# Kernel tuning notes

Measured on AMD Instinct MI355X. Metric: run time of the kernel, lower is better.

## Reference

```python
import jax, jax.numpy as jnp
import numpy as np

N_CAR, N_LIGHT, N_STOP = 180000, 10000, 10000
N = N_CAR + N_LIGHT + N_STOP
E = 6_400_000

# LossConfig defaults
LAMBDA_RECON, LAMBDA_RULE, LAMBDA_ATTN, LAMBDA_REG = 1.0, 0.5, 0.3, 1e-4
W_ATTN_GAT, W_ATTN_RULE = 0.5, 0.5
VIOL_THRESH = 0.5


def setup_inputs() -> dict:
    key = jax.random.key(0)
    ks = jax.random.split(key, 8)
    eps = 1e-6
    model_scores = jnp.clip(jax.random.uniform(ks[0], (N_CAR,), jnp.float32), eps, 1.0 - eps)
    rule_scores = jnp.clip(jax.random.uniform(ks[1], (N_CAR,), jnp.float32), eps, 1.0 - eps)
    alpha_gat = jax.random.uniform(ks[2], (E,), jnp.float32)
    beta_rule = jax.random.uniform(ks[3], (N_CAR,), jnp.float32)
    src = jax.random.randint(ks[4], (E,), 0, N)
    dst = jax.random.randint(ks[5], (E,), 0, N)
    edge_index = jnp.stack([src, dst], axis=0)
    # cars first (type 0), then lights (1), then stop lines (2)
    entity_types = jnp.concatenate([
        jnp.zeros((N_CAR,), jnp.int32),
        jnp.ones((N_LIGHT,), jnp.int32),
        jnp.full((N_STOP,), 2, jnp.int32),
    ])
    param0 = jax.random.normal(ks[6], (4096, 4096), jnp.float32) * 0.02
    param1 = jax.random.normal(ks[7], (4096, 4096), jnp.float32) * 0.02
    return {
        "model_scores": model_scores, "rule_scores": rule_scores,
        "alpha_gat": alpha_gat, "beta_rule": beta_rule,
        "edge_index": edge_index, "entity_types": entity_types,
        "param0": param0, "param1": param1,
    }


def _bce(x, t):
    # torch F.binary_cross_entropy clamps log at -100
    log_x = jnp.clip(jnp.log(x), -100.0)
    log_1mx = jnp.clip(jnp.log1p(-x), -100.0)
    return jnp.mean(-(t * log_x + (1.0 - t) * log_1mx))


def _gat_attn_loss(alpha_gat, edge_index, entity_types, violation_mask):
    src, dst = edge_index[0], edge_index[1]
    dst_t = entity_types[dst]
    rule_edge = (dst_t == 1) | (dst_t == 2)
    masked = jnp.where(rule_edge, alpha_gat, -jnp.inf)
    # fused segment-max over source nodes replaces the per-car Python loop
    seg_max = jax.ops.segment_max(masked, src, num_segments=N)  # [N]
    car_ids = jnp.nonzero(entity_types == 0, size=N_CAR)[0]      # [N_car]
    max_attn = seg_max[car_ids]                                  # [N_car]
    valid = jnp.isfinite(max_attn) & violation_mask             # cars w/ rule neighbor
    safe = jnp.where(valid, max_attn, 0.0)
    total = jnp.sum(jnp.where(valid, (1.0 - safe) ** 2, 0.0))
    cnt = jnp.sum(valid)
    return jnp.where(cnt > 0, total / jnp.maximum(cnt, 1).astype(total.dtype), 0.0)


def _rule_attn_loss(beta_rule, violation_mask):
    total = jnp.sum(jnp.where(violation_mask, (1.0 - beta_rule) ** 2, 0.0))
    cnt = jnp.sum(violation_mask)
    return jnp.where(cnt > 0, total / jnp.maximum(cnt, 1).astype(total.dtype), 0.0)


@jax.jit
def reference(model_scores, rule_scores, alpha_gat, beta_rule, edge_index, entity_types, param0, param1):
    L_recon = _bce(model_scores, rule_scores)
    L_rule = jnp.mean((model_scores - rule_scores) ** 2)
    violation_mask = rule_scores > VIOL_THRESH
    any_viol = jnp.any(violation_mask)
    L_attn_gat = jnp.where(any_viol, _gat_attn_loss(alpha_gat, edge_index, entity_types, violation_mask), 0.0)
    L_attn_rule = jnp.where(any_viol, _rule_attn_loss(beta_rule, violation_mask), 0.0)
    L_attn = W_ATTN_GAT * L_attn_gat + W_ATTN_RULE * L_attn_rule
    L_reg = jnp.sum(param0 ** 2) + jnp.sum(param1 ** 2)
    L_total = (LAMBDA_RECON * L_recon + LAMBDA_RULE * L_rule
               + LAMBDA_ATTN * L_attn + LAMBDA_REG * L_reg)
    num_violations = jnp.sum(violation_mask).astype(jnp.float32)
    return (L_total, L_recon, L_rule, L_attn, L_attn_gat, L_attn_rule, L_reg, num_violations)
```

## Files before the change

kernel.cpp:

```cpp
#include <hip/hip_runtime.h>

#define N_CAR   180000
#define NE      6400000
#define P_ELEMS (4096 * 4096)
#define P4      (P_ELEMS / 4)

#define REG_BLOCKS   2048
#define REG_THREADS  (REG_BLOCKS * 256)
#define REG_ITERS    (P4 / REG_THREADS)

#define EDGE_BLOCKS  2048
#define EDGE_THREADS (EDGE_BLOCKS * 256)
#define EDGE_QUADS   (NE / 4)

#define CAR_BLOCKS   ((N_CAR + 255) / 256)

typedef float f4 __attribute__((ext_vector_type(4)));
typedef int   i4 __attribute__((ext_vector_type(4)));


__device__ __forceinline__ float wave_reduce_sum(float s) {
#pragma unroll
    for (int off = 32; off > 0; off >>= 1) s += __shfl_down(s, off, 64);
    return s;
}

__global__ void __launch_bounds__(256) init_kernel(i4* __restrict__ segmax4) {
    int i = blockIdx.x * blockDim.x + threadIdx.x;
    const int NINF = (int)0xFF800000u;
    if (i < N_CAR / 4) {
        i4 v = {NINF, NINF, NINF, NINF};
        segmax4[i] = v;
    }
}

__global__ void __launch_bounds__(256) fused_kernel(const i4* __restrict__ src4,
                                                    const i4* __restrict__ dst4,
                                                    const f4* __restrict__ alpha4,
                                                    int* __restrict__ segmax,
                                                    const f4* __restrict__ p0,
                                                    const f4* __restrict__ p1,
                                                    float* __restrict__ regpart) {
    __shared__ float red[4];
    int slot = blockIdx.x & 1;
    int g    = blockIdx.x >> 1;
    if (slot == 0) {
        int t = g * 256 + threadIdx.x;
        f4 acc = {0.f, 0.f, 0.f, 0.f};
#pragma unroll
        for (int k = 0; k < REG_ITERS; ++k) {
            f4 a = p0[t + k * REG_THREADS];
            acc += a * a;
        }
#pragma unroll
        for (int k = 0; k < REG_ITERS; ++k) {
            f4 b = p1[t + k * REG_THREADS];
            acc += b * b;
        }
        float s = (acc.x + acc.y) + (acc.z + acc.w);
        s = wave_reduce_sum(s);
        int wave = threadIdx.x >> 6;
        int lane = threadIdx.x & 63;
        if (lane == 0) red[wave] = s;
        __syncthreads();
        if (threadIdx.x == 0)
            regpart[g] = red[0] + red[1] + red[2] + red[3];
    } else {
        int t = g * 256 + threadIdx.x;
        for (int q = t; q < EDGE_QUADS; q += EDGE_THREADS) {
            i4 d  = dst4[q];
            i4 sv = src4[q];
            f4 a  = alpha4[q];
            if (d.x >= N_CAR && sv.x < N_CAR) atomicMax(&segmax[sv.x], __float_as_int(a.x));
            if (d.y >= N_CAR && sv.y < N_CAR) atomicMax(&segmax[sv.y], __float_as_int(a.y));
            if (d.z >= N_CAR && sv.z < N_CAR) atomicMax(&segmax[sv.z], __float_as_int(a.z));
            if (d.w >= N_CAR && sv.w < N_CAR) atomicMax(&segmax[sv.w], __float_as_int(a.w));
        }
    }
}

__global__ void __launch_bounds__(256) car_kernel(const float* __restrict__ ms,
                                                  const float* __restrict__ rs,
                                                  const float* __restrict__ beta,
                                                  const int* __restrict__ segmax,
                                                  float* __restrict__ carpart) {
    int i = blockIdx.x * blockDim.x + threadIdx.x;
    float vals[6] = {0.f, 0.f, 0.f, 0.f, 0.f, 0.f};
    if (i < N_CAR) {
        float x = ms[i];
        float t = rs[i];
        float lx  = fmaxf(logf(x), -100.0f);
        float l1x = fmaxf(log1pf(-x), -100.0f);
        vals[0] = -(t * lx + (1.0f - t) * l1x);
        float df = x - t;
        vals[1] = df * df;
        if (t > 0.5f) {
            vals[2] = 1.0f;
            float b = beta[i];
            vals[3] = (1.0f - b) * (1.0f - b);
            float m = __int_as_float(segmax[i]);
            if (m >= 0.0f) {
                vals[4] = (1.0f - m) * (1.0f - m);
                vals[5] = 1.0f;
            }
        }
    }
    __shared__ float red[4][6];
    int wave = threadIdx.x >> 6;
    int lane = threadIdx.x & 63;
#pragma unroll
    for (int k = 0; k < 6; ++k) {
        float s = wave_reduce_sum(vals[k]);
        if (lane == 0) red[wave][k] = s;
    }
    __syncthreads();
    if (threadIdx.x == 0) {
#pragma unroll
        for (int k = 0; k < 6; ++k)
            carpart[blockIdx.x * 6 + k] = red[0][k] + red[1][k] + red[2][k] + red[3][k];
    }
}

__global__ void __launch_bounds__(256) finalize_kernel(const float* __restrict__ regpart,
                                                       const float* __restrict__ carpart,
                                                       float* __restrict__ out) {
    int tid = threadIdx.x;
    float rsum = 0.0f;
    for (int i = tid; i < REG_BLOCKS; i += 256) rsum += regpart[i];
    float c[6] = {0.f, 0.f, 0.f, 0.f, 0.f, 0.f};
    for (int r = tid; r < CAR_BLOCKS; r += 256) {
#pragma unroll
        for (int k = 0; k < 6; ++k) c[k] += carpart[r * 6 + k];
    }
    __shared__ float red[4][7];
    int wave = tid >> 6;
    int lane = tid & 63;
    {
        float s = wave_reduce_sum(rsum);
        if (lane == 0) red[wave][6] = s;
    }
#pragma unroll
    for (int k = 0; k < 6; ++k) {
        float s = wave_reduce_sum(c[k]);
        if (lane == 0) red[wave][k] = s;
    }
    __syncthreads();
    if (tid == 0) {
        float tot[7];
#pragma unroll
        for (int k = 0; k < 7; ++k)
            tot[k] = red[0][k] + red[1][k] + red[2][k] + red[3][k];
        const float inv_ncar = 1.0f / (float)N_CAR;
        float L_recon = tot[0] * inv_ncar;
        float L_rule  = tot[1] * inv_ncar;
        float vc      = tot[2];
        float L_attn_rule = (vc > 0.0f) ? tot[3] / vc : 0.0f;
        float gat_cnt = tot[5];
        float L_attn_gat = (vc > 0.0f && gat_cnt > 0.0f) ? tot[4] / gat_cnt : 0.0f;
        float L_attn = 0.5f * L_attn_gat + 0.5f * L_attn_rule;
        float L_reg  = tot[6];
        float L_total = 1.0f * L_recon + 0.5f * L_rule + 0.3f * L_attn + 1e-4f * L_reg;
        out[0] = L_total;
        out[1] = L_recon;
        out[2] = L_rule;
        out[3] = L_attn;
        out[4] = L_attn_gat;
        out[5] = L_attn_rule;
        out[6] = L_reg;
        out[7] = vc;
    }
}

extern "C" void kernel_launch(void* const* d_in, const int* in_sizes, int n_in,
                              void* d_out, int out_size, void* d_ws, size_t ws_size,
                              hipStream_t stream) {
    const float* model_scores = (const float*)d_in[0];
    const float* rule_scores  = (const float*)d_in[1];
    const float* alpha_gat    = (const float*)d_in[2];
    const float* beta_rule    = (const float*)d_in[3];
    const int*   edge_index   = (const int*)d_in[4];
    const float* param0       = (const float*)d_in[6];
    const float* param1       = (const float*)d_in[7];
    float* out = (float*)d_out;

    int*   segmax  = (int*)d_ws;
    float* regpart = (float*)d_ws + N_CAR;
    float* carpart = regpart + REG_BLOCKS;

    const int* src = edge_index;
    const int* dst = edge_index + NE;

    init_kernel<<<(N_CAR / 4 + 255) / 256, 256, 0, stream>>>((i4*)segmax);
    fused_kernel<<<REG_BLOCKS + EDGE_BLOCKS, 256, 0, stream>>>(
        (const i4*)src, (const i4*)dst, (const f4*)alpha_gat, segmax,
        (const f4*)param0, (const f4*)param1, regpart);
    car_kernel<<<CAR_BLOCKS, 256, 0, stream>>>(model_scores, rule_scores,
                                               beta_rule, segmax, carpart);
    finalize_kernel<<<1, 256, 0, stream>>>(regpart, carpart, out);
}
```

Baseline: 233.2 us.

## Merge reg and edge work per block, fold finalize into car kernel via atomics

Each of the 4096 blocks now does its slice of the parameter sum of squares and then its slice of the edge atomicMax scan, instead of splitting blocks between the two jobs. The partial sums are accumulated with global atomicAdd. A last-block ticket in the car kernel computes the final losses, which removes the separate finalize launch. This saves one kernel launch and the partial-sum arrays, but it adds atomic contention on the accumulators and makes the float summation order nondeterministic.

Measured after the change: 293.9 us. +26.0%, slower.

```diff
diff --git a/kernel.cpp b/kernel.cpp
--- a/kernel.cpp
+++ b/kernel.cpp
@@ -5,12 +5,9 @@
 #define P_ELEMS (4096 * 4096)
 #define P4      (P_ELEMS / 4)
 
-#define REG_BLOCKS   2048
-#define REG_THREADS  (REG_BLOCKS * 256)
-#define REG_ITERS    (P4 / REG_THREADS)
-
-#define EDGE_BLOCKS  2048
-#define EDGE_THREADS (EDGE_BLOCKS * 256)
+#define WORK_BLOCKS  4096
+#define WORK_T       (WORK_BLOCKS * 256)
+#define REG_ITERS    (P4 / WORK_T)
 #define EDGE_QUADS   (NE / 4)
 
 #define CAR_BLOCKS   ((N_CAR + 255) / 256)
@@ -25,65 +22,65 @@
     return s;
 }
 
-__global__ void __launch_bounds__(256) init_kernel(i4* __restrict__ segmax4) {
+__global__ void __launch_bounds__(256) init_kernel(i4* __restrict__ segmax4,
+                                                   float* __restrict__ acc,
+                                                   int* __restrict__ done) {
     int i = blockIdx.x * blockDim.x + threadIdx.x;
     const int NINF = (int)0xFF800000u;
     if (i < N_CAR / 4) {
         i4 v = {NINF, NINF, NINF, NINF};
         segmax4[i] = v;
     }
+    if (i < 7) acc[i] = 0.0f;
+    if (i == 7) *done = 0;
 }
 
-__global__ void __launch_bounds__(256) fused_kernel(const i4* __restrict__ src4,
-                                                    const i4* __restrict__ dst4,
-                                                    const f4* __restrict__ alpha4,
-                                                    int* __restrict__ segmax,
-                                                    const f4* __restrict__ p0,
-                                                    const f4* __restrict__ p1,
-                                                    float* __restrict__ regpart) {
+__global__ void __launch_bounds__(256) work_kernel(const i4* __restrict__ src4,
+                                                   const i4* __restrict__ dst4,
+                                                   const f4* __restrict__ alpha4,
+                                                   int* __restrict__ segmax,
+                                                   const f4* __restrict__ p0,
+                                                   const f4* __restrict__ p1,
+                                                   float* __restrict__ acc) {
+    int t = blockIdx.x * 256 + threadIdx.x;
+    f4 a = {0.f, 0.f, 0.f, 0.f};
+#pragma unroll
+    for (int k = 0; k < REG_ITERS; ++k) {
+        f4 v = p0[t + k * WORK_T];
+        a += v * v;
+    }
+#pragma unroll
+    for (int k = 0; k < REG_ITERS; ++k) {
+        f4 v = p1[t + k * WORK_T];
+        a += v * v;
+    }
+    float s = (a.x + a.y) + (a.z + a.w);
+    s = wave_reduce_sum(s);
     __shared__ float red[4];
-    int slot = blockIdx.x & 1;
-    int g    = blockIdx.x >> 1;
-    if (slot == 0) {
-        int t = g * 256 + threadIdx.x;
-        f4 acc = {0.f, 0.f, 0.f, 0.f};
-#pragma unroll
-        for (int k = 0; k < REG_ITERS; ++k) {
-            f4 a = p0[t + k * REG_THREADS];
-            acc += a * a;
-        }
-#pragma unroll
-        for (int k = 0; k < REG_ITERS; ++k) {
-            f4 b = p1[t + k * REG_THREADS];
-            acc += b * b;
-        }
-        float s = (acc.x + acc.y) + (acc.z + acc.w);
-        s = wave_reduce_sum(s);
-        int wave = threadIdx.x >> 6;
-        int lane = threadIdx.x & 63;
-        if (lane == 0) red[wave] = s;
-        __syncthreads();
-        if (threadIdx.x == 0)
-            regpart[g] = red[0] + red[1] + red[2] + red[3];
-    } else {
-        int t = g * 256 + threadIdx.x;
-        for (int q = t; q < EDGE_QUADS; q += EDGE_THREADS) {
-            i4 d  = dst4[q];
-            i4 sv = src4[q];
-            f4 a  = alpha4[q];
-            if (d.x >= N_CAR && sv.x < N_CAR) atomicMax(&segmax[sv.x], __float_as_int(a.x));
-            if (d.y >= N_CAR && sv.y < N_CAR) atomicMax(&segmax[sv.y], __float_as_int(a.y));
-            if (d.z >= N_CAR && sv.z < N_CAR) atomicMax(&segmax[sv.z], __float_as_int(a.z));
-            if (d.w >= N_CAR && sv.w < N_CAR) atomicMax(&segmax[sv.w], __float_as_int(a.w));
-        }
+    int wave = threadIdx.x >> 6;
+    int lane = threadIdx.x & 63;
+    if (lane == 0) red[wave] = s;
+    __syncthreads();
+    if (threadIdx.x == 0)
+        atomicAdd(&acc[6], red[0] + red[1] + red[2] + red[3]);
+    for (int q = t; q < EDGE_QUADS; q += WORK_T) {
+        i4 d  = dst4[q];
+        i4 sv = src4[q];
+        f4 al = alpha4[q];
+        if (d.x >= N_CAR && sv.x < N_CAR) atomicMax(&segmax[sv.x], __float_as_int(al.x));
+        if (d.y >= N_CAR && sv.y < N_CAR) atomicMax(&segmax[sv.y], __float_as_int(al.y));
+        if (d.z >= N_CAR && sv.z < N_CAR) atomicMax(&segmax[sv.z], __float_as_int(al.z));
+        if (d.w >= N_CAR && sv.w < N_CAR) atomicMax(&segmax[sv.w], __float_as_int(al.w));
     }
 }
 
-__global__ void __launch_bounds__(256) car_kernel(const float* __restrict__ ms,
-                                                  const float* __restrict__ rs,
-                                                  const float* __restrict__ beta,
-                                                  const int* __restrict__ segmax,
-                                                  float* __restrict__ carpart) {
+__global__ void __launch_bounds__(256) carfin_kernel(const float* __restrict__ ms,
+                                                     const float* __restrict__ rs,
+                                                     const float* __restrict__ beta,
+                                                     const int* __restrict__ segmax,
+                                                     float* __restrict__ acc,
+                                                     int* __restrict__ done,
+                                                     float* __restrict__ out) {
     int i = blockIdx.x * blockDim.x + threadIdx.x;
     float vals[6] = {0.f, 0.f, 0.f, 0.f, 0.f, 0.f};
     if (i < N_CAR) {
@@ -117,57 +114,33 @@
     if (threadIdx.x == 0) {
 #pragma unroll
         for (int k = 0; k < 6; ++k)
-            carpart[blockIdx.x * 6 + k] = red[0][k] + red[1][k] + red[2][k] + red[3][k];
-    }
-}
-
-__global__ void __launch_bounds__(256) finalize_kernel(const float* __restrict__ regpart,
-                                                       const float* __restrict__ carpart,
-                                                       float* __restrict__ out) {
-    int tid = threadIdx.x;
-    float rsum = 0.0f;
-    for (int i = tid; i < REG_BLOCKS; i += 256) rsum += regpart[i];
-    float c[6] = {0.f, 0.f, 0.f, 0.f, 0.f, 0.f};
-    for (int r = tid; r < CAR_BLOCKS; r += 256) {
+            atomicAdd(&acc[k], red[0][k] + red[1][k] + red[2][k] + red[3][k]);
+        __threadfence();
+        int ticket = atomicAdd(done, 1);
+        if (ticket == CAR_BLOCKS - 1) {
+            float tot[7];
 #pragma unroll
-        for (int k = 0; k < 6; ++k) c[k] += carpart[r * 6 + k];
-    }
-    __shared__ float red[4][7];
-    int wave = tid >> 6;
-    int lane = tid & 63;
-    {
-        float s = wave_reduce_sum(rsum);
-        if (lane == 0) red[wave][6] = s;
-    }
-#pragma unroll
-    for (int k = 0; k < 6; ++k) {
-        float s = wave_reduce_sum(c[k]);
-        if (lane == 0) red[wave][k] = s;
-    }
-    __syncthreads();
-    if (tid == 0) {
-        float tot[7];
-#pragma unroll
-        for (int k = 0; k < 7; ++k)
-            tot[k] = red[0][k] + red[1][k] + red[2][k] + red[3][k];
-        const float inv_ncar = 1.0f / (float)N_CAR;
-        float L_recon = tot[0] * inv_ncar;
-        float L_rule  = tot[1] * inv_ncar;
-        float vc      = tot[2];
-        float L_attn_rule = (vc > 0.0f) ? tot[3] / vc : 0.0f;
-        float gat_cnt = tot[5];
-        float L_attn_gat = (vc > 0.0f && gat_cnt > 0.0f) ? tot[4] / gat_cnt : 0.0f;
-        float L_attn = 0.5f * L_attn_gat + 0.5f * L_attn_rule;
-        float L_reg  = tot[6];
-        float L_total = 1.0f * L_recon + 0.5f * L_rule + 0.3f * L_attn + 1e-4f * L_reg;
-        out[0] = L_total;
-        out[1] = L_recon;
-        out[2] = L_rule;
-        out[3] = L_attn;
-        out[4] = L_attn_gat;
-        out[5] = L_attn_rule;
-        out[6] = L_reg;
-        out[7] = vc;
+            for (int k = 0; k < 7; ++k)
+                tot[k] = atomicAdd(&acc[k], 0.0f);
+            const float inv_ncar = 1.0f / (float)N_CAR;
+            float L_recon = tot[0] * inv_ncar;
+            float L_rule  = tot[1] * inv_ncar;
+            float vc      = tot[2];
+            float L_attn_rule = (vc > 0.0f) ? tot[3] / vc : 0.0f;
+            float gat_cnt = tot[5];
+            float L_attn_gat = (vc > 0.0f && gat_cnt > 0.0f) ? tot[4] / gat_cnt : 0.0f;
+            float L_attn = 0.5f * L_attn_gat + 0.5f * L_attn_rule;
+            float L_reg  = tot[6];
+            float L_total = 1.0f * L_recon + 0.5f * L_rule + 0.3f * L_attn + 1e-4f * L_reg;
+            out[0] = L_total;
+            out[1] = L_recon;
+            out[2] = L_rule;
+            out[3] = L_attn;
+            out[4] = L_attn_gat;
+            out[5] = L_attn_rule;
+            out[6] = L_reg;
+            out[7] = vc;
+        }
     }
 }
 
@@ -183,18 +156,17 @@
     const float* param1       = (const float*)d_in[7];
     float* out = (float*)d_out;
 
-    int*   segmax  = (int*)d_ws;
-    float* regpart = (float*)d_ws + N_CAR;
-    float* carpart = regpart + REG_BLOCKS;
+    int*   segmax = (int*)d_ws;
+    float* acc    = (float*)d_ws + N_CAR;
+    int*   done   = (int*)d_ws + N_CAR + 7;
 
     const int* src = edge_index;
     const int* dst = edge_index + NE;
 
-    init_kernel<<<(N_CAR / 4 + 255) / 256, 256, 0, stream>>>((i4*)segmax);
-    fused_kernel<<<REG_BLOCKS + EDGE_BLOCKS, 256, 0, stream>>>(
+    init_kernel<<<(N_CAR / 4 + 255) / 256, 256, 0, stream>>>((i4*)segmax, acc, done);
+    work_kernel<<<WORK_BLOCKS, 256, 0, stream>>>(
         (const i4*)src, (const i4*)dst, (const f4*)alpha_gat, segmax,
-        (const f4*)param0, (const f4*)param1, regpart);
-    car_kernel<<<CAR_BLOCKS, 256, 0, stream>>>(model_scores, rule_scores,
-                                               beta_rule, segmax, carpart);
-    finalize_kernel<<<1, 256, 0, stream>>>(regpart, carpart, out);
+        (const f4*)param0, (const f4*)param1, acc);
+    carfin_kernel<<<CAR_BLOCKS, 256, 0, stream>>>(model_scores, rule_scores,
+                                                  beta_rule, segmax, acc, done, out);
 }
```
